# Kernel tuning notes

Measured on AMD Instinct MI355X. Metric: run time of the kernel, lower is better.

Reference implementation:

```python
import math
import jax, jax.numpy as jnp
import numpy as np

NUM_HEADS = 16
HEAD_DIM = 64
NB_FEATURES = 256
EPS = 1e-06
DATA_NORM = HEAD_DIM ** (-0.25)


def setup_inputs() -> dict:
    key = jax.random.key(0)
    ks = jax.random.split(key, 5)
    B, N, C = 4, 4096, 1024
    x = jax.random.normal(ks[0], (B, N, C), dtype=jnp.float32)
    w_qkv = jax.random.normal(ks[1], (C, 3 * C), dtype=jnp.float32) * (C ** -0.5)
    b_qkv = jnp.zeros((3 * C,), dtype=jnp.float32)
    w_out = jax.random.normal(ks[2], (C, C), dtype=jnp.float32) * (C ** -0.5)
    b_out = jnp.zeros((C,), dtype=jnp.float32)
    proj = jax.random.normal(ks[3], (NUM_HEADS, NB_FEATURES, HEAD_DIM), dtype=jnp.float32)
    proj = proj / jnp.linalg.norm(proj, axis=-1, keepdims=True)  # F.normalize(dim=-1)
    return {"x": x, "w_qkv": w_qkv, "b_qkv": b_qkv, "w_out": w_out, "b_out": b_out,
            "proj_matrix": proj}


def _feature_map(x, proj):
    # x: [b,h,n,d], proj: [h,m,d] -> [b,h,n,m]
    x = x * DATA_NORM
    x_proj = jnp.einsum('bhnd,hmd->bhnm', x, proj)
    sq_norms = 0.5 * jnp.sum(x * x, axis=-1, keepdims=True)
    x_proj = x_proj - sq_norms
    x_proj = x_proj - jnp.max(x_proj, axis=-1, keepdims=True)
    return (jnp.exp(x_proj) + EPS) / math.sqrt(NB_FEATURES)


def reference(x, w_qkv, b_qkv, w_out, b_out, proj_matrix):
    B, N, C = x.shape
    h, d = NUM_HEADS, HEAD_DIM
    qkv = x @ w_qkv + b_qkv                     # [B,N,3C]
    q, k, v = jnp.split(qkv, 3, axis=-1)
    to_heads = lambda z: z.reshape(B, N, h, d).transpose(0, 2, 1, 3)  # [B,h,N,d]
    q, k, v = to_heads(q), to_heads(k), to_heads(v)

    q_prime = _feature_map(q, proj_matrix)      # [B,h,N,m]
    k_prime = _feature_map(k, proj_matrix)      # [B,h,N,m]

    k_sum = jnp.sum(k_prime, axis=2)                          # [B,h,m]
    kv = jnp.einsum('bhnm,bhnd->bhmd', k_prime, v)            # [B,h,m,d]
    numerator = jnp.einsum('bhnm,bhmd->bhnd', q_prime, kv)    # [B,h,N,d]
    denominator = jnp.einsum('bhnm,bhm->bhn', q_prime, k_sum) + EPS
    out = numerator / denominator[..., None]

    out = out.transpose(0, 2, 1, 3).reshape(B, N, C)
    return out @ w_out + b_out
```

## Files before the change

kernel.cpp:

```cpp
#include <hip/hip_runtime.h>
#include <hip/hip_bf16.h>
#include <stdint.h>


#define DN 0.35355339059327379f
#define EPSF 1e-6f
#define INV_SQRT_M 0.0625f

typedef __attribute__((ext_vector_type(8))) short bf16x8;
typedef __attribute__((ext_vector_type(4))) float f32x4;

static __device__ __forceinline__ short f2bf(float f) {
    __hip_bfloat16 h = __float2bfloat16(f);
    return *(short*)&h;
}
static __device__ __forceinline__ void gload16(const void* g, void* l) {
    __builtin_amdgcn_global_load_lds(
        (const __attribute__((address_space(1))) void*)g,
        (__attribute__((address_space(3))) void*)l,
        16, 0, 0);
}

__global__ __launch_bounds__(256) void conv_x(const float* __restrict__ X,
                                              short* __restrict__ Xb) {
    int i = blockIdx.x * 256 + threadIdx.x;
    float4 v = ((const float4*)X)[i];
    short4 o;
    o.x = f2bf(v.x); o.y = f2bf(v.y); o.z = f2bf(v.z); o.w = f2bf(v.w);
    ((short4*)Xb)[i] = o;
}

__global__ __launch_bounds__(256) void convt_w(const float* __restrict__ W,
                                               short* __restrict__ WT,
                                               int K, int NN) {
    __shared__ short tile[64][66];
    int t = threadIdx.x;
    int k0 = blockIdx.y * 64, n0 = blockIdx.x * 64;
    for (int i = t; i < 4096; i += 256) {
        int r = i >> 6, c = i & 63;
        tile[r][c] = f2bf(W[(size_t)(k0 + r) * NN + n0 + c]);
    }
    __syncthreads();
    for (int i = t; i < 4096; i += 256) {
        int r = i >> 6, c = i & 63;
        WT[(size_t)(n0 + r) * K + k0 + c] = tile[c][r];
    }
}

__global__ __launch_bounds__(256) void conv_proj(const float* __restrict__ proj,
                                                 short* __restrict__ pjb) {
    int e = blockIdx.x * 256 + threadIdx.x;
    int m = (e >> 6) & 255, d = e & 63;
    int base = e & ~63;
    pjb[base + (d ^ ((m & 7) << 3))] = f2bf(proj[e]);
}

__device__ __forceinline__ void gemm_core128(const short* __restrict__ A,
                                             const short* __restrict__ BT,
                                             int rowBase, int colBase,
                                             char* smem, f32x4 acc[4][4]) {
    const int K = 1024;
    int t = threadIdx.x, lane = t & 63, w = t >> 6;
    int li = lane & 15, g = lane >> 4;
    int wm = w >> 1, wn = w & 1;

    const char* aSrc[4]; const char* bSrc[4]; int aOff[4];
#pragma unroll
    for (int c = 0; c < 4; ++c) {
        int idx = c * 256 + t;
        int r = idx >> 3, s = t & 7;
        aOff[c] = idx * 16;
        aSrc[c] = (const char*)(A + (size_t)(rowBase + r) * K + ((s ^ (r & 7)) * 8));
        bSrc[c] = (const char*)(BT + (size_t)(colBase + r) * K + ((s ^ (r & 7)) * 8));
    }
#pragma unroll
    for (int m = 0; m < 4; ++m)
#pragma unroll
        for (int n = 0; n < 4; ++n) acc[m][n] = (f32x4){0.f, 0.f, 0.f, 0.f};

#pragma unroll
    for (int c = 0; c < 4; ++c) {
        gload16(aSrc[c], smem + aOff[c]);
        gload16(bSrc[c], smem + 16384 + aOff[c]);
    }

    int swz = (li & 7) << 4;

    for (int tt = 0; tt < 16; ++tt) {
        int cur = tt & 1;
        if (tt < 15) {
            char* d = smem + (cur ^ 1) * 32768;
#pragma unroll
            for (int c = 0; c < 4; ++c) {
                gload16(aSrc[c] + (size_t)(tt + 1) * 128, d + aOff[c]);
                gload16(bSrc[c] + (size_t)(tt + 1) * 128, d + 16384 + aOff[c]);
            }
            asm volatile("s_waitcnt vmcnt(8)" ::: "memory");
        } else {
            asm volatile("s_waitcnt vmcnt(0)" ::: "memory");
        }
        __builtin_amdgcn_sched_barrier(0);
        __builtin_amdgcn_s_barrier();
        __builtin_amdgcn_sched_barrier(0);
        __builtin_amdgcn_s_setprio(1);
        const char* bA = smem + cur * 32768;
        const char* bB = bA + 16384;
#pragma unroll
        for (int ks = 0; ks < 2; ++ks) {
            int kb = ks * 64 + g * 16;
            bf16x8 af[4], bv[4];
#pragma unroll
            for (int m = 0; m < 4; ++m)
                af[m] = *(const bf16x8*)(bA + (wm * 64 + m * 16 + li) * 128 + (kb ^ swz));
#pragma unroll
            for (int n = 0; n < 4; ++n)
                bv[n] = *(const bf16x8*)(bB + (wn * 64 + n * 16 + li) * 128 + (kb ^ swz));
#pragma unroll
            for (int m = 0; m < 4; ++m)
#pragma unroll
                for (int n = 0; n < 4; ++n)
                    acc[m][n] = __builtin_amdgcn_mfma_f32_16x16x32_bf16(
                        af[m], bv[n], acc[m][n], 0, 0, 0);
        }
        __builtin_amdgcn_s_setprio(0);
        __builtin_amdgcn_sched_barrier(0);
        __builtin_amdgcn_s_barrier();
        __builtin_amdgcn_sched_barrier(0);
    }
}

__global__ __launch_bounds__(256, 2) void mfma_gemm_qkv(
        const short* __restrict__ A, const short* __restrict__ BT,
        const float* __restrict__ bias,
        short* __restrict__ Qh, short* __restrict__ Kh, short* __restrict__ Vt) {
    __shared__ __align__(16) char smem[65536];
    int t = threadIdx.x, lane = t & 63, w = t >> 6;
    int li = lane & 15, g = lane >> 4, wm = w >> 1, wn = w & 1;
    int lin = blockIdx.x;
    int sz = (lin & 7) * 384 + (lin >> 3);
    int bx = sz % 24, by = sz / 24;
    int rowBase = by * 128, colBase = bx * 128;

    f32x4 acc[4][4];
    gemm_core128(A, BT, rowBase, colBase, smem, acc);

    float bcol[4];
#pragma unroll
    for (int n = 0; n < 4; ++n) bcol[n] = bias[colBase + wn * 64 + n * 16 + li];
    int whichB = colBase >> 10;

    if (whichB == 2) {
#pragma unroll
        for (int n = 0; n < 4; ++n) {
            int gc = colBase + wn * 64 + n * 16 + li;
            int hh = (gc & 1023) >> 6, dd = gc & 63;
#pragma unroll
            for (int m = 0; m < 4; ++m) {
                int gr0 = rowBase + wm * 64 + m * 16 + g * 4;
                int b = gr0 >> 12, nn0 = gr0 & 4095;
                short4 o;
                o.x = f2bf(acc[m][n][0] + bcol[n]);
                o.y = f2bf(acc[m][n][1] + bcol[n]);
                o.z = f2bf(acc[m][n][2] + bcol[n]);
                o.w = f2bf(acc[m][n][3] + bcol[n]);
                int nsw = (nn0 & ~63) | ((nn0 & 63) ^ ((dd & 7) << 3));
                *(short4*)&Vt[((size_t)(b * 16 + hh) * 64 + dd) * 4096 + nsw] = o;
            }
        }
    } else {
        short* dst = (whichB == 0) ? Qh : Kh;
        int hh = ((colBase + wn * 64) & 1023) >> 6;
        float* wreg = (float*)(smem + w * 8704);
#pragma unroll
        for (int r = 0; r < 2; ++r) {
#pragma unroll
            for (int mi = 0; mi < 2; ++mi)
#pragma unroll
                for (int n = 0; n < 4; ++n)
#pragma unroll
                    for (int jj = 0; jj < 4; ++jj)
                        wreg[(mi * 16 + g * 4 + jj) * 68 + n * 16 + li] =
                            (acc[2 * r + mi][n][jj] + bcol[n]) * DN;
            int row = lane >> 1, h2 = lane & 1;
            int tok = rowBase + wm * 64 + r * 32 + row;
            int b = tok >> 12, nn = tok & 4095;
            size_t base = ((size_t)(b * 16 + hh) * 4096 + nn) * 64;
#pragma unroll
            for (int k = 0; k < 4; ++k) {
                float4 v0 = *(const float4*)&wreg[row * 68 + h2 * 32 + k * 8];
                float4 v1 = *(const float4*)&wreg[row * 68 + h2 * 32 + k * 8 + 4];
                bf16x8 ov;
                ov[0] = f2bf(v0.x); ov[1] = f2bf(v0.y);
                ov[2] = f2bf(v0.z); ov[3] = f2bf(v0.w);
                ov[4] = f2bf(v1.x); ov[5] = f2bf(v1.y);
                ov[6] = f2bf(v1.z); ov[7] = f2bf(v1.w);
                int dgrp = (h2 * 4 + k) ^ (tok & 7);
                *(bf16x8*)&dst[base + dgrp * 8] = ov;
            }
        }
    }
}

__global__ __launch_bounds__(256, 2) void mfma_gemm_out(
        const short* __restrict__ A, const short* __restrict__ BT,
        const float* __restrict__ bias, float* __restrict__ C) {
    __shared__ __align__(16) char smem[65536];
    int t = threadIdx.x, lane = t & 63, w = t >> 6;
    int li = lane & 15, g = lane >> 4, wm = w >> 1, wn = w & 1;
    int lin = blockIdx.x;
    int sz = (lin & 7) * 128 + (lin >> 3);
    int bx = sz & 7, by = sz >> 3;
    int rowBase = by * 128, colBase = bx * 128;

    f32x4 acc[4][4];
    gemm_core128(A, BT, rowBase, colBase, smem, acc);

    float bcol[4];
#pragma unroll
    for (int n = 0; n < 4; ++n) bcol[n] = bias[colBase + wn * 64 + n * 16 + li];
    float* wreg = (float*)(smem + w * 8704);
#pragma unroll
    for (int r = 0; r < 2; ++r) {
#pragma unroll
        for (int mi = 0; mi < 2; ++mi)
#pragma unroll
            for (int n = 0; n < 4; ++n)
#pragma unroll
                for (int jj = 0; jj < 4; ++jj)
                    wreg[(mi * 16 + g * 4 + jj) * 68 + n * 16 + li] =
                        acc[2 * r + mi][n][jj] + bcol[n];
        int row = lane >> 1, h2 = lane & 1;
        int gr = rowBase + wm * 64 + r * 32 + row;
        float* cp = C + (size_t)gr * 1024 + colBase + wn * 64 + h2 * 32;
#pragma unroll
        for (int k = 0; k < 8; ++k)
            *(float4*)&cp[k * 4] = *(const float4*)&wreg[row * 68 + h2 * 32 + k * 4];
    }
}

__global__ __launch_bounds__(256) void fmap_mfma(const short* __restrict__ Kh,
                                                 const short* __restrict__ Vt,
                                                 const short* __restrict__ pjb,
                                                 float* __restrict__ kvpart,
                                                 float* __restrict__ kspart) {
    int bh = blockIdx.y, ch = blockIdx.x, h = bh & 15;
    int t = threadIdx.x, lane = t & 63, w = t >> 6;
    int g = lane >> 4, li = lane & 15;
    __shared__ __align__(16) short pj[256 * 64];
    __shared__ __align__(16) short kt[64 * 64];
    __shared__ __align__(16) short vt[64 * 64];
    __shared__ __align__(16) short Pl[4][64 * 40];
    __shared__ __align__(16) float maxw[4][64];

    {
        const short* psrc = pjb + (size_t)h * 16384;
#pragma unroll
        for (int c2 = 0; c2 < 8; ++c2) {
            int c = 8 * w + c2;
            gload16(psrc + c * 512 + lane * 8, pj + c * 512);
        }
    }

    f32x4 acc[4][4];
#pragma unroll
    for (int i = 0; i < 4; ++i)
#pragma unroll
        for (int j = 0; j < 4; ++j) acc[i][j] = (f32x4){0.f, 0.f, 0.f, 0.f};
    float ksacc[4] = {0.f, 0.f, 0.f, 0.f};

    const short* kbase = Kh + ((size_t)bh * 4096 + ch * 512) * 64;
    const short* vbase = Vt + (size_t)bh * 64 * 4096 + ch * 512;
    int swz = (li & 7) << 4;

    for (int tile = 0; tile < 8; ++tile) {
        __syncthreads();
#pragma unroll
        for (int c2 = 0; c2 < 2; ++c2) {
            int c = 2 * w + c2;
            gload16(kbase + (size_t)(tile * 64) * 64 + c * 512 + lane * 8,
                    kt + c * 512);
            int d = 8 * c + (lane >> 3);
            gload16(vbase + (size_t)d * 4096 + tile * 64 + (lane & 7) * 8,
                    vt + c * 512);
        }
        __syncthreads();

        f32x4 sacc[4][4];
#pragma unroll
        for (int i = 0; i < 4; ++i)
#pragma unroll
            for (int j = 0; j < 4; ++j) sacc[i][j] = (f32x4){0.f, 0.f, 0.f, 0.f};
#pragma unroll
        for (int ks = 0; ks < 2; ++ks) {
            int kb = ks * 64 + g * 16;
            bf16x8 afr[4], bfr[4];
#pragma unroll
            for (int ni = 0; ni < 4; ++ni)
                afr[ni] = *(const bf16x8*)((const char*)kt +
                           (16 * ni + li) * 128 + (kb ^ swz));
#pragma unroll
            for (int mi = 0; mi < 4; ++mi)
                bfr[mi] = *(const bf16x8*)((const char*)pj +
                           (64 * w + 16 * mi + li) * 128 + (kb ^ swz));
#pragma unroll
            for (int ni = 0; ni < 4; ++ni)
#pragma unroll
                for (int mi = 0; mi < 4; ++mi)
                    sacc[ni][mi] = __builtin_amdgcn_mfma_f32_16x16x32_bf16(
                        afr[ni], bfr[mi], sacc[ni][mi], 0, 0, 0);
        }

        float mxl[4][4];
#pragma unroll
        for (int ni = 0; ni < 4; ++ni)
#pragma unroll
            for (int jj = 0; jj < 4; ++jj) {
                float m0 = fmaxf(sacc[ni][0][jj], sacc[ni][1][jj]);
                float m1 = fmaxf(sacc[ni][2][jj], sacc[ni][3][jj]);
                mxl[ni][jj] = fmaxf(m0, m1);
            }
#pragma unroll
        for (int off = 1; off <= 8; off <<= 1)
#pragma unroll
            for (int ni = 0; ni < 4; ++ni)
#pragma unroll
                for (int jj = 0; jj < 4; ++jj)
                    mxl[ni][jj] = fmaxf(mxl[ni][jj], __shfl_xor(mxl[ni][jj], off));
        if (li == 0) {
#pragma unroll
            for (int ni = 0; ni < 4; ++ni)
                *(float4*)&maxw[w][16 * ni + 4 * g] =
                    make_float4(mxl[ni][0], mxl[ni][1], mxl[ni][2], mxl[ni][3]);
        }
        __syncthreads();

#pragma unroll
        for (int hf = 0; hf < 2; ++hf) {
#pragma unroll
            for (int ni2 = 0; ni2 < 2; ++ni2) {
                int ni = 2 * hf + ni2;
                float4 a0 = *(const float4*)&maxw[0][16 * ni + 4 * g];
                float4 a1 = *(const float4*)&maxw[1][16 * ni + 4 * g];
                float4 a2 = *(const float4*)&maxw[2][16 * ni + 4 * g];
                float4 a3 = *(const float4*)&maxw[3][16 * ni + 4 * g];
                float mm[4];
                mm[0] = fmaxf(fmaxf(a0.x, a1.x), fmaxf(a2.x, a3.x));
                mm[1] = fmaxf(fmaxf(a0.y, a1.y), fmaxf(a2.y, a3.y));
                mm[2] = fmaxf(fmaxf(a0.z, a1.z), fmaxf(a2.z, a3.z));
                mm[3] = fmaxf(fmaxf(a0.w, a1.w), fmaxf(a2.w, a3.w));
#pragma unroll
                for (int mi = 0; mi < 4; ++mi) {
                    float p0 = (__expf(sacc[ni][mi][0] - mm[0]) + EPSF) * INV_SQRT_M;
                    float p1 = (__expf(sacc[ni][mi][1] - mm[1]) + EPSF) * INV_SQRT_M;
                    float p2 = (__expf(sacc[ni][mi][2] - mm[2]) + EPSF) * INV_SQRT_M;
                    float p3 = (__expf(sacc[ni][mi][3] - mm[3]) + EPSF) * INV_SQRT_M;
                    ksacc[mi] += (p0 + p1) + (p2 + p3);
                    uint32_t u0 = (uint32_t)(uint16_t)f2bf(p0) |
                                  ((uint32_t)(uint16_t)f2bf(p1) << 16);
                    uint32_t u1 = (uint32_t)(uint16_t)f2bf(p2) |
                                  ((uint32_t)(uint16_t)f2bf(p3) << 16);
                    int m_l = 16 * mi + li;
                    *(uint2*)((char*)Pl[w] + m_l * 80 + 32 * ni2 + 8 * g) =
                        make_uint2(u0, u1);
                }
            }
#pragma unroll
            for (int mi = 0; mi < 4; ++mi) {
                bf16x8 pa = *(const bf16x8*)((const char*)Pl[w] +
                             (16 * mi + li) * 80 + 16 * g);
#pragma unroll
                for (int di = 0; di < 4; ++di) {
                    bf16x8 bv = *(const bf16x8*)((const char*)vt +
                                 (16 * di + li) * 128 + ((64 * hf + 16 * g) ^ swz));
                    acc[mi][di] = __builtin_amdgcn_mfma_f32_16x16x32_bf16(
                        pa, bv, acc[mi][di], 0, 0, 0);
                }
            }
        }
    }

#pragma unroll
    for (int mi = 0; mi < 4; ++mi) {
        ksacc[mi] += __shfl_xor(ksacc[mi], 16);
        ksacc[mi] += __shfl_xor(ksacc[mi], 32);
    }
    if (lane < 16) {
#pragma unroll
        for (int mi = 0; mi < 4; ++mi)
            kspart[(bh * 8 + ch) * 256 + 64 * w + 16 * mi + li] = ksacc[mi];
    }
    float* kvb = kvpart + (size_t)(bh * 8 + ch) * 16384;
#pragma unroll
    for (int mi = 0; mi < 4; ++mi)
#pragma unroll
        for (int di = 0; di < 4; ++di) {
            int d = 16 * di + li, m0 = 64 * w + 16 * mi + 4 * g;
            *(float4*)&kvb[d * 256 + m0] =
                make_float4(acc[mi][di][0], acc[mi][di][1],
                            acc[mi][di][2], acc[mi][di][3]);
        }
}

__global__ __launch_bounds__(256) void reduce_kv(const float* __restrict__ kvpart,
                                                 const float* __restrict__ kspart,
                                                 short* __restrict__ kvsT) {
    int bh = blockIdx.y, bx = blockIdx.x, t = threadIdx.x;
    if (bx < 4) {
#pragma unroll
        for (int i = 0; i < 16; ++i) {
            int idx = t + i * 256;
            int d = 16 * bx + (idx >> 8), m = idx & 255;
            float s = 0.f;
            size_t base = ((size_t)(bh * 8) * 64 + d) * 256 + m;
#pragma unroll
            for (int c = 0; c < 8; ++c) s += kvpart[base + (size_t)c * 16384];
            int widx = (m & 128) + ((m & 127) ^ ((d & 7) << 3));
            kvsT[((size_t)bh * 80 + d) * 256 + widx] = f2bf(s);
        }
    } else {
        float s = 0.f;
#pragma unroll
        for (int c = 0; c < 8; ++c) s += kspart[((bh * 8 + c) << 8) + t];
        kvsT[((size_t)bh * 80 + 64) * 256 + t] = f2bf(s);
        for (int i = t; i < 15 * 256; i += 256) {
            int r = 65 + (i >> 8), cc = i & 255;
            kvsT[((size_t)bh * 80 + r) * 256 + cc] = 0;
        }
    }
}

__global__ __launch_bounds__(256) void contract_mfma(
        const short* __restrict__ Qh,
        const short* __restrict__ pjb,
        const short* __restrict__ kvsT,
        short* __restrict__ attn) {
    int bh = blockIdx.y, rb = blockIdx.x, h = bh & 15, b = bh >> 4;
    int t = threadIdx.x, lane = t & 63, w = t >> 6;
    __shared__ __align__(16) short qs[64 * 64];
    __shared__ __align__(16) short pj[128 * 64];
    __shared__ __align__(16) short Pl[64 * 128];
    __shared__ __align__(16) short kvl[80 * 128];

    {
        const short* src = Qh + ((size_t)bh * 4096 + rb * 64) * 64;
#pragma unroll
        for (int c2 = 0; c2 < 2; ++c2) {
            int c = 2 * w + c2;
            gload16(src + (c * 8 + (lane >> 3)) * 64 + (lane & 7) * 8,
                    qs + c * 512);
        }
    }

    f32x4 acc5[5];
#pragma unroll
    for (int i = 0; i < 5; ++i) acc5[i] = (f32x4){0.f, 0.f, 0.f, 0.f};

    int g = lane >> 4, li = lane & 15;

    for (int half = 0; half < 2; ++half) {
        __syncthreads();
        const short* psrc = pjb + (size_t)h * 16384 + half * 8192;
#pragma unroll
        for (int c2 = 0; c2 < 4; ++c2) {
            int c = 4 * w + c2;
            gload16(psrc + (c * 8 + (lane >> 3)) * 64 + (lane & 7) * 8,
                    pj + c * 512);
        }
        const short* ksrc = kvsT + (size_t)bh * 80 * 256 + half * 128;
#pragma unroll
        for (int c2 = 0; c2 < 5; ++c2) {
            int c = 5 * w + c2;
            gload16(ksrc + (c * 4 + (lane >> 4)) * 256 + (lane & 15) * 8,
                    kvl + c * 512);
        }
        __syncthreads();

        f32x4 sacc[2][4];
#pragma unroll
        for (int mi = 0; mi < 2; ++mi)
#pragma unroll
            for (int ni = 0; ni < 4; ++ni) sacc[mi][ni] = (f32x4){0.f, 0.f, 0.f, 0.f};
#pragma unroll
        for (int ks = 0; ks < 2; ++ks) {
            int kbyte = ks * 64 + g * 16;
            bf16x8 afr[2], bfr[4];
#pragma unroll
            for (int mi = 0; mi < 2; ++mi) {
                int mr = 32 * w + 16 * mi + li;
                afr[mi] = *(const bf16x8*)((const char*)pj +
                           mr * 128 + (kbyte ^ ((mr & 7) << 4)));
            }
#pragma unroll
            for (int ni = 0; ni < 4; ++ni) {
                int qr = 16 * ni + li;
                bfr[ni] = *(const bf16x8*)((const char*)qs +
                           qr * 128 + (kbyte ^ ((qr & 7) << 4)));
            }
#pragma unroll
            for (int mi = 0; mi < 2; ++mi)
#pragma unroll
                for (int ni = 0; ni < 4; ++ni)
                    sacc[mi][ni] = __builtin_amdgcn_mfma_f32_16x16x32_bf16(
                        afr[mi], bfr[ni], sacc[mi][ni], 0, 0, 0);
        }

#pragma unroll
        for (int mi = 0; mi < 2; ++mi) {
            int m0 = 32 * w + 16 * mi + 4 * g;
#pragma unroll
            for (int ni = 0; ni < 4; ++ni) {
                int row = 16 * ni + li;
                float e0 = (__expf(sacc[mi][ni][0]) + EPSF) * INV_SQRT_M;
                float e1 = (__expf(sacc[mi][ni][1]) + EPSF) * INV_SQRT_M;
                float e2 = (__expf(sacc[mi][ni][2]) + EPSF) * INV_SQRT_M;
                float e3 = (__expf(sacc[mi][ni][3]) + EPSF) * INV_SQRT_M;
                uint32_t u0 = (uint32_t)(uint16_t)f2bf(e0) |
                              ((uint32_t)(uint16_t)f2bf(e1) << 16);
                uint32_t u1 = (uint32_t)(uint16_t)f2bf(e2) |
                              ((uint32_t)(uint16_t)f2bf(e3) << 16);
                int byte = row * 256 + ((m0 * 2) ^ ((row & 7) << 4));
                *(uint2*)((char*)Pl + byte) = make_uint2(u0, u1);
            }
        }
        __syncthreads();

        int rowA = 16 * w + li;
        int abase = rowA * 256;
        int asw = (rowA & 7) << 4;
#pragma unroll
        for (int ks = 0; ks < 4; ++ks) {
            int kbyte = ks * 64 + g * 16;
            bf16x8 pa = *(const bf16x8*)((const char*)Pl + abase + (kbyte ^ asw));
#pragma unroll
            for (int ni = 0; ni < 5; ++ni) {
                int rowB = 16 * ni + li;
                bf16x8 bv = *(const bf16x8*)((const char*)kvl +
                             rowB * 256 + (kbyte ^ ((rowB & 7) << 4)));
                acc5[ni] = __builtin_amdgcn_mfma_f32_16x16x32_bf16(
                    pa, bv, acc5[ni], 0, 0, 0);
            }
        }
    }

    float dj[4];
#pragma unroll
    for (int jj = 0; jj < 4; ++jj)
        dj[jj] = __shfl(acc5[4][jj], lane & 48) + EPSF;
#pragma unroll
    for (int ni = 0; ni < 4; ++ni) {
        int d = 16 * ni + li;
#pragma unroll
        for (int jj = 0; jj < 4; ++jj) {
            int n = rb * 64 + 16 * w + 4 * g + jj;
            attn[((size_t)b * 4096 + n) * 1024 + h * 64 + d] =
                f2bf(acc5[ni][jj] / dj[jj]);
        }
    }
}

extern "C" void kernel_launch(void* const* d_in, const int* in_sizes, int n_in,
                              void* d_out, int out_size, void* d_ws, size_t ws_size,
                              hipStream_t stream) {
    const float* x      = (const float*)d_in[0];
    const float* w_qkv  = (const float*)d_in[1];
    const float* b_qkv  = (const float*)d_in[2];
    const float* w_out  = (const float*)d_in[3];
    const float* b_out  = (const float*)d_in[4];
    const float* proj   = (const float*)d_in[5];
    float* out = (float*)d_out;

    char* w = (char*)d_ws;
    short* xb     = (short*)(w);
    short* wqT    = (short*)(w + 33554432);
    short* wOT    = (short*)(w + 39845888);
    short* Qh     = (short*)(w + 41943040);
    short* Kh     = (short*)(w + 75497472);
    short* Vt     = (short*)(w + 109051904);
    float* kvpart = (float*)(w);
    float* kspart = (float*)(w + 142606336);
    short* kvsT   = (short*)(w + 143130624);
    short* pjb    = (short*)(w + 145752064);
    short* attn   = Kh;

    conv_x<<<dim3(16384), 256, 0, stream>>>(x, xb);
    convt_w<<<dim3(48, 16), 256, 0, stream>>>(w_qkv, wqT, 1024, 3072);
    convt_w<<<dim3(16, 16), 256, 0, stream>>>(w_out, wOT, 1024, 1024);
    conv_proj<<<dim3(1024), 256, 0, stream>>>(proj, pjb);
    mfma_gemm_qkv<<<dim3(3072), 256, 0, stream>>>(xb, wqT, b_qkv, Qh, Kh, Vt);
    fmap_mfma<<<dim3(8, 64), 256, 0, stream>>>(Kh, Vt, pjb, kvpart, kspart);
    reduce_kv<<<dim3(5, 64), 256, 0, stream>>>(kvpart, kspart, kvsT);
    contract_mfma<<<dim3(64, 64), 256, 0, stream>>>(Qh, pjb, kvsT, attn);
    mfma_gemm_out<<<dim3(1024), 256, 0, stream>>>(attn, wOT, b_out, out);
}
```

Measured before the change: 333.3 us.

## Use triple-buffered BK=32 GEMM pipeline and register-prefetch K/V tiles in fmap

The shared GEMM core now uses 32-wide K tiles with a three-stage LDS ring and a new XOR swizzle, in place of 64-wide double buffering. This cuts LDS per block from 64KB to 48KB, so launch bounds rise to three blocks per CU for more occupancy. The grouped block-index swizzle for L2 locality is removed. The fmap kernel prefetches the next K/V tile into registers during compute and writes it to LDS afterwards, hiding global load latency at the cost of extra registers and a barrier.

```diff
diff --git a/kernel.cpp b/kernel.cpp
--- a/kernel.cpp
+++ b/kernel.cpp
@@ -64,38 +64,53 @@
     int li = lane & 15, g = lane >> 4;
     int wm = w >> 1, wn = w & 1;
 
-    const char* aSrc[4]; const char* bSrc[4]; int aOff[4];
-#pragma unroll
-    for (int c = 0; c < 4; ++c) {
+    const char* aSrc[2]; const char* bSrc[2]; int dOff[2];
+#pragma unroll
+    for (int c = 0; c < 2; ++c) {
         int idx = c * 256 + t;
-        int r = idx >> 3, s = t & 7;
-        aOff[c] = idx * 16;
-        aSrc[c] = (const char*)(A + (size_t)(rowBase + r) * K + ((s ^ (r & 7)) * 8));
-        bSrc[c] = (const char*)(BT + (size_t)(colBase + r) * K + ((s ^ (r & 7)) * 8));
+        int r = idx >> 2, s = idx & 3;
+        dOff[c] = idx * 16;
+        int sg = (s ^ ((r >> 1) & 3)) * 16;
+        aSrc[c] = (const char*)(A + (size_t)(rowBase + r) * K) + sg;
+        bSrc[c] = (const char*)(BT + (size_t)(colBase + r) * K) + sg;
     }
 #pragma unroll
     for (int m = 0; m < 4; ++m)
 #pragma unroll
         for (int n = 0; n < 4; ++n) acc[m][n] = (f32x4){0.f, 0.f, 0.f, 0.f};
 
-#pragma unroll
-    for (int c = 0; c < 4; ++c) {
-        gload16(aSrc[c], smem + aOff[c]);
-        gload16(bSrc[c], smem + 16384 + aOff[c]);
-    }
-
-    int swz = (li & 7) << 4;
-
-    for (int tt = 0; tt < 16; ++tt) {
-        int cur = tt & 1;
-        if (tt < 15) {
-            char* d = smem + (cur ^ 1) * 32768;
-#pragma unroll
-            for (int c = 0; c < 4; ++c) {
-                gload16(aSrc[c] + (size_t)(tt + 1) * 128, d + aOff[c]);
-                gload16(bSrc[c] + (size_t)(tt + 1) * 128, d + 16384 + aOff[c]);
-            }
+    int fsw = (li >> 1) & 3;
+    int offA[4], offB[4];
+#pragma unroll
+    for (int m = 0; m < 4; ++m) {
+        offA[m] = (wm * 64 + m * 16 + li) * 64 + ((g ^ fsw) << 4);
+        offB[m] = (wn * 64 + m * 16 + li) * 64 + ((g ^ fsw) << 4);
+    }
+
+#pragma unroll
+    for (int tt = 0; tt < 2; ++tt) {
+        char* d = smem + tt * 16384;
+#pragma unroll
+        for (int c = 0; c < 2; ++c) {
+            gload16(aSrc[c] + tt * 64, d + dOff[c]);
+            gload16(bSrc[c] + tt * 64, d + 8192 + dOff[c]);
+        }
+    }
+
+    int cur = 0, s3 = 2;
+    for (int tt = 0; tt < 32; ++tt) {
+        if (tt < 30) {
+            char* d = smem + s3 * 16384;
+            size_t kb = (size_t)(tt + 2) * 64;
+#pragma unroll
+            for (int c = 0; c < 2; ++c) {
+                gload16(aSrc[c] + kb, d + dOff[c]);
+                gload16(bSrc[c] + kb, d + 8192 + dOff[c]);
+            }
+            s3 = (s3 == 2) ? 0 : s3 + 1;
             asm volatile("s_waitcnt vmcnt(8)" ::: "memory");
+        } else if (tt == 30) {
+            asm volatile("s_waitcnt vmcnt(4)" ::: "memory");
         } else {
             asm volatile("s_waitcnt vmcnt(0)" ::: "memory");
         }
@@ -103,42 +118,36 @@
         __builtin_amdgcn_s_barrier();
         __builtin_amdgcn_sched_barrier(0);
         __builtin_amdgcn_s_setprio(1);
-        const char* bA = smem + cur * 32768;
-        const char* bB = bA + 16384;
-#pragma unroll
-        for (int ks = 0; ks < 2; ++ks) {
-            int kb = ks * 64 + g * 16;
-            bf16x8 af[4], bv[4];
-#pragma unroll
-            for (int m = 0; m < 4; ++m)
-                af[m] = *(const bf16x8*)(bA + (wm * 64 + m * 16 + li) * 128 + (kb ^ swz));
+        const char* bA = smem + cur * 16384;
+        const char* bB = bA + 8192;
+        bf16x8 af[4], bv[4];
+#pragma unroll
+        for (int m = 0; m < 4; ++m) af[m] = *(const bf16x8*)(bA + offA[m]);
+#pragma unroll
+        for (int n = 0; n < 4; ++n) bv[n] = *(const bf16x8*)(bB + offB[n]);
+#pragma unroll
+        for (int m = 0; m < 4; ++m)
 #pragma unroll
             for (int n = 0; n < 4; ++n)
-                bv[n] = *(const bf16x8*)(bB + (wn * 64 + n * 16 + li) * 128 + (kb ^ swz));
-#pragma unroll
-            for (int m = 0; m < 4; ++m)
-#pragma unroll
-                for (int n = 0; n < 4; ++n)
-                    acc[m][n] = __builtin_amdgcn_mfma_f32_16x16x32_bf16(
-                        af[m], bv[n], acc[m][n], 0, 0, 0);
-        }
+                acc[m][n] = __builtin_amdgcn_mfma_f32_16x16x32_bf16(
+                    af[m], bv[n], acc[m][n], 0, 0, 0);
         __builtin_amdgcn_s_setprio(0);
         __builtin_amdgcn_sched_barrier(0);
         __builtin_amdgcn_s_barrier();
         __builtin_amdgcn_sched_barrier(0);
-    }
-}
-
-__global__ __launch_bounds__(256, 2) void mfma_gemm_qkv(
+        cur = (cur == 2) ? 0 : cur + 1;
+    }
+}
+
+__global__ __launch_bounds__(256, 3) void mfma_gemm_qkv(
         const short* __restrict__ A, const short* __restrict__ BT,
         const float* __restrict__ bias,
         short* __restrict__ Qh, short* __restrict__ Kh, short* __restrict__ Vt) {
-    __shared__ __align__(16) char smem[65536];
+    __shared__ __align__(16) char smem[49152];
     int t = threadIdx.x, lane = t & 63, w = t >> 6;
     int li = lane & 15, g = lane >> 4, wm = w >> 1, wn = w & 1;
     int lin = blockIdx.x;
-    int sz = (lin & 7) * 384 + (lin >> 3);
-    int bx = sz % 24, by = sz / 24;
+    int bx = lin % 24, by = lin / 24;
     int rowBase = by * 128, colBase = bx * 128;
 
     f32x4 acc[4][4];
@@ -201,15 +210,14 @@
     }
 }
 
-__global__ __launch_bounds__(256, 2) void mfma_gemm_out(
+__global__ __launch_bounds__(256, 3) void mfma_gemm_out(
         const short* __restrict__ A, const short* __restrict__ BT,
         const float* __restrict__ bias, float* __restrict__ C) {
-    __shared__ __align__(16) char smem[65536];
+    __shared__ __align__(16) char smem[49152];
     int t = threadIdx.x, lane = t & 63, w = t >> 6;
     int li = lane & 15, g = lane >> 4, wm = w >> 1, wn = w & 1;
     int lin = blockIdx.x;
-    int sz = (lin & 7) * 128 + (lin >> 3);
-    int bx = sz & 7, by = sz >> 3;
+    int bx = lin & 7, by = lin >> 3;
     int rowBase = by * 128, colBase = bx * 128;
 
     f32x4 acc[4][4];
@@ -252,6 +260,9 @@
     __shared__ __align__(16) short Pl[4][64 * 40];
     __shared__ __align__(16) float maxw[4][64];
 
+    const short* kbase = Kh + ((size_t)bh * 4096 + ch * 512) * 64;
+    const short* vbase = Vt + (size_t)bh * 64 * 4096 + ch * 512;
+
     {
         const short* psrc = pjb + (size_t)h * 16384;
 #pragma unroll
@@ -259,7 +270,15 @@
             int c = 8 * w + c2;
             gload16(psrc + c * 512 + lane * 8, pj + c * 512);
         }
-    }
+#pragma unroll
+        for (int c2 = 0; c2 < 2; ++c2) {
+            int c = 2 * w + c2;
+            gload16(kbase + c * 512 + lane * 8, kt + c * 512);
+            int d = 8 * c + (lane >> 3);
+            gload16(vbase + (size_t)d * 4096 + (lane & 7) * 8, vt + c * 512);
+        }
+    }
+    __syncthreads();
 
     f32x4 acc[4][4];
 #pragma unroll
@@ -268,22 +287,19 @@
         for (int j = 0; j < 4; ++j) acc[i][j] = (f32x4){0.f, 0.f, 0.f, 0.f};
     float ksacc[4] = {0.f, 0.f, 0.f, 0.f};
 
-    const short* kbase = Kh + ((size_t)bh * 4096 + ch * 512) * 64;
-    const short* vbase = Vt + (size_t)bh * 64 * 4096 + ch * 512;
     int swz = (li & 7) << 4;
 
     for (int tile = 0; tile < 8; ++tile) {
-        __syncthreads();
-#pragma unroll
-        for (int c2 = 0; c2 < 2; ++c2) {
-            int c = 2 * w + c2;
-            gload16(kbase + (size_t)(tile * 64) * 64 + c * 512 + lane * 8,
-                    kt + c * 512);
-            int d = 8 * c + (lane >> 3);
-            gload16(vbase + (size_t)d * 4096 + tile * 64 + (lane & 7) * 8,
-                    vt + c * 512);
-        }
-        __syncthreads();
+        bf16x8 rk0, rk1, rv0, rv1;
+        if (tile < 7) {
+            int c0 = 2 * w, c1 = 2 * w + 1;
+            size_t kof = (size_t)((tile + 1) * 64) * 64;
+            rk0 = *(const bf16x8*)(kbase + kof + c0 * 512 + lane * 8);
+            rk1 = *(const bf16x8*)(kbase + kof + c1 * 512 + lane * 8);
+            int d0 = 8 * c0 + (lane >> 3), d1 = 8 * c1 + (lane >> 3);
+            rv0 = *(const bf16x8*)(vbase + (size_t)d0 * 4096 + (tile + 1) * 64 + (lane & 7) * 8);
+            rv1 = *(const bf16x8*)(vbase + (size_t)d1 * 4096 + (tile + 1) * 64 + (lane & 7) * 8);
+        }
 
         f32x4 sacc[4][4];
 #pragma unroll
@@ -377,6 +393,15 @@
                 }
             }
         }
+        __syncthreads();
+        if (tile < 7) {
+            int c0 = 2 * w, c1 = 2 * w + 1;
+            *(bf16x8*)((char*)kt + c0 * 1024 + lane * 16) = rk0;
+            *(bf16x8*)((char*)kt + c1 * 1024 + lane * 16) = rk1;
+            *(bf16x8*)((char*)vt + c0 * 1024 + lane * 16) = rv0;
+            *(bf16x8*)((char*)vt + c1 * 1024 + lane * 16) = rv1;
+            __syncthreads();
+        }
     }
 
 #pragma unroll
```

Result: slower. 345.1 us (+3.5%).
